# Kernel optimization log

Measured on AMD Instinct MI355X. Metric: run time of the kernel, lower is better.

## Reference

```python
import jax, jax.numpy as jnp
import numpy as np

B, IN, O = 256, 512, 10
STRUCTURES = list(range(32, 257, 32))  # 8 neuron structures
REPS, N_ACT = 4, 4


def _build_hidden_ids():
    ids = []
    i = 0
    # activation-major, then repetition, then structure (matches build_model_ids)
    for _ in range(N_ACT * REPS):
        for s in STRUCTURES:
            ids += [i] * s
            i += 1
    return np.asarray(ids, dtype=np.int32), i


def setup_inputs() -> dict:
    ids, M = _build_hidden_ids()
    H = len(ids)  # 18432
    k = jax.random.split(jax.random.key(0), 5)
    x = jax.random.normal(k[0], (B, IN), dtype=jnp.float32)
    hidden_w = jax.random.normal(k[1], (H, IN), dtype=jnp.float32) / np.sqrt(IN)
    hidden_b = jax.random.normal(k[2], (H,), dtype=jnp.float32) * 0.02
    out_w = jax.random.normal(k[3], (O, H), dtype=jnp.float32) * 0.05
    out_b = jax.random.normal(k[4], (M, O), dtype=jnp.float32) * 0.02
    return {"x": x, "hidden_w": hidden_w, "hidden_b": hidden_b,
            "out_w": out_w, "out_b": out_b,
            "hidden_ids": jnp.asarray(ids)}


_ACTS = [jax.nn.relu, jnp.tanh, jax.nn.sigmoid, lambda t: t]


def reference(x, hidden_w, hidden_b, out_w, out_b, hidden_ids):
    # hidden layer: [B, H]
    h = x @ hidden_w.T + hidden_b
    # per-activation contiguous splits (equal size H // n_act)
    chunks = jnp.split(h, N_ACT, axis=1)
    a = jnp.concatenate([f(c) for f, c in zip(_ACTS, chunks)], axis=1)  # [B, H]
    # per-hidden-neuron contribution to each output unit: [B, H, O]
    contrib = a[:, :, None] * out_w.T[None, :, :]
    M = out_b.shape[0]
    # segment-reduce hidden neurons into their model id: [M, B, O] -> [B, M, O]
    agg = jax.ops.segment_sum(contrib.transpose(1, 0, 2), hidden_ids, num_segments=M)
    return agg.transpose(1, 0, 2) + out_b[None, :, :]
```

## Files before the change

### kernel.cpp

```cpp
#include <hip/hip_runtime.h>
#include <hip/hip_bf16.h>

typedef __bf16 bf16x8 __attribute__((ext_vector_type(8)));
typedef float floatx4 __attribute__((ext_vector_type(4)));

#define BATCH 256
#define INDIM 512
#define ODIM 10
#define HTOT 18432
#define NMODEL 128
#define HTILE 64
#define BTILE 64
#define BK 32
#define ACT_CHUNK 4608
#define WCNT (HTOT * INDIM)
#define XCNT (BATCH * INDIM)
#define NJPG (HTOT / 32)

#define GLOAD_LDS(gp, lp) __builtin_amdgcn_global_load_lds( \
    (const __attribute__((address_space(1))) unsigned int*)(const void*)(gp), \
    (__attribute__((address_space(3))) unsigned int*)(lp), 16, 0, 0)

__device__ __forceinline__ unsigned pk2(float a, float b) {
    unsigned ua = __float_as_uint(a);
    ua = (ua + 0x7fffu + ((ua >> 16) & 1u)) >> 16;
    unsigned ub = __float_as_uint(b);
    ub = (ub + 0x7fffu + ((ub >> 16) & 1u)) >> 16;
    return ua | (ub << 16);
}

__device__ __forceinline__ float apply_act(float h, int aidx) {
    if (aidx == 0) return fmaxf(h, 0.f);
    if (aidx == 1) return 1.f - 2.f / (1.f + __expf(2.f * h));
    if (aidx == 2) return 1.f / (1.f + __expf(-h));
    return h;
}

__global__ __launch_bounds__(256) void convert_kernel(
    const float* __restrict__ hw, const float* __restrict__ x,
    unsigned short* __restrict__ dst)
{
    size_t i = (size_t)(blockIdx.x * 256 + threadIdx.x) * 8;
    const float* src = (i < (size_t)WCNT) ? hw + i : x + (i - WCNT);
    floatx4 v0 = *(const floatx4*)src;
    floatx4 v1 = *(const floatx4*)(src + 4);
    uint4 o;
    o.x = pk2(v0[0], v0[1]); o.y = pk2(v0[2], v0[3]);
    o.z = pk2(v1[0], v1[1]); o.w = pk2(v1[2], v1[3]);
    *(uint4*)(dst + i) = o;
}

__global__ __launch_bounds__(256, 5) void mlp_kernel(
    const unsigned short* __restrict__ wbf, const unsigned short* __restrict__ xbf,
    const float* __restrict__ hidden_b, const float* __restrict__ out_w,
    float* __restrict__ part)
{
    __shared__ __align__(16) unsigned short xs[BTILE * BK];
    __shared__ __align__(16) unsigned short wsx[HTILE * BK];
    __shared__ float wtile[ODIM * HTILE];
    __shared__ float btile[HTILE];

    const int tid = threadIdx.x;
    const int bid = blockIdx.x;
    const int jb = bid >> 2, bb = bid & 3;
    const int j0 = jb * HTILE;
    const int b0 = bb * BTILE;
    const int lane = tid & 63;
    const int wvid = tid >> 6;
    const int r = lane & 15;
    const int g = lane >> 4;

    for (int i = tid; i < ODIM * HTILE; i += 256)
        wtile[i] = out_w[(i >> 6) * HTOT + j0 + (i & 63)];
    if (tid < HTILE) btile[tid] = hidden_b[j0 + tid];

    floatx4 acc[4];
    #pragma unroll
    for (int jt = 0; jt < 4; jt++) acc[jt] = (floatx4)0.f;

    const int srow = wvid * 16 + (lane >> 2);
    const int scol = (lane & 3) * 8;
    const unsigned short* gw = wbf + (size_t)(j0 + srow) * INDIM + scol;
    const unsigned short* gx = xbf + (size_t)(b0 + srow) * INDIM + scol;
    unsigned short* lw = &wsx[wvid * 16 * BK];
    unsigned short* lx = &xs[wvid * 16 * BK];

    for (int kk = 0; kk < INDIM; kk += BK) {
        GLOAD_LDS(gw + kk, lw);
        GLOAD_LDS(gx + kk, lx);
        __syncthreads();
        bf16x8 bfr = *(const bf16x8*)&xs[(wvid * 16 + r) * BK + g * 8];
        #pragma unroll
        for (int jt = 0; jt < 4; jt++) {
            bf16x8 af = *(const bf16x8*)&wsx[(jt * 16 + r) * BK + g * 8];
            acc[jt] = __builtin_amdgcn_mfma_f32_16x16x32_bf16(af, bfr, acc[jt], 0, 0, 0);
        }
        __syncthreads();
    }

    const int aidx = j0 / ACT_CHUNK;
    const int b = b0 + wvid * 16 + r;

    #pragma unroll
    for (int jp = 0; jp < 2; jp++) {
        const int jpg = (j0 >> 5) + jp;
        float a[2][4];
        #pragma unroll
        for (int h = 0; h < 2; h++) {
            int jt = jp * 2 + h;
            #pragma unroll
            for (int q = 0; q < 4; q++)
                a[h][q] = apply_act(acc[jt][q] + btile[jt * 16 + g * 4 + q], aidx);
        }
        #pragma unroll
        for (int o = 0; o < ODIM; o++) {
            float p = 0.f;
            #pragma unroll
            for (int h = 0; h < 2; h++) {
                int jt = jp * 2 + h;
                const float* wr = &wtile[o * HTILE + jt * 16 + g * 4];
                p += a[h][0] * wr[0] + a[h][1] * wr[1] + a[h][2] * wr[2] + a[h][3] * wr[3];
            }
            p += __shfl_xor(p, 16, 64);
            p += __shfl_xor(p, 32, 64);
            if (lane < 16)
                part[((size_t)jpg * ODIM + o) * BATCH + b] = p;
        }
    }
}

__global__ __launch_bounds__(256) void finalize_kernel(
    const float* __restrict__ part, const float* __restrict__ out_b,
    float* __restrict__ out)
{
    const int mo = blockIdx.x;
    const int m = mo / ODIM, o = mo - m * ODIM;
    const int b = threadIdx.x;
    const int rep = m >> 3, idx = m & 7;
    const int jp0 = rep * 36 + (idx * (idx + 1)) / 2;
    const int cnt = idx + 1;

    float s = out_b[mo];
    for (int c = 0; c < cnt; c++)
        s += part[((size_t)(jp0 + c) * ODIM + o) * BATCH + b];
    out[((size_t)b * NMODEL + m) * ODIM + o] = s;
}

extern "C" void kernel_launch(void* const* d_in, const int* in_sizes, int n_in,
                              void* d_out, int out_size, void* d_ws, size_t ws_size,
                              hipStream_t stream) {
    const float* x   = (const float*)d_in[0];
    const float* hw  = (const float*)d_in[1];
    const float* hb  = (const float*)d_in[2];
    const float* ow  = (const float*)d_in[3];
    const float* ob  = (const float*)d_in[4];
    float* out = (float*)d_out;

    unsigned short* wbf = (unsigned short*)d_ws;
    unsigned short* xbf = wbf + WCNT;
    float* part = (float*)d_ws + (WCNT + XCNT) / 2;

    convert_kernel<<<(WCNT + XCNT) / 8 / 256, 256, 0, stream>>>(hw, x, wbf);
    mlp_kernel<<<(HTOT / HTILE) * (BATCH / BTILE), 256, 0, stream>>>(wbf, xbf, hb, ow, part);
    finalize_kernel<<<NMODEL * ODIM, 256, 0, stream>>>(part, ob, out);
}
```

Before: 115.9 us.

## Widen K tile, use 2x2 wave MFMA tiling and XOR-swizzled LDS layout

Raises the K step from 32 to 128, so the GEMM loop runs 4 iterations instead of 16 and barrier overhead drops. Each wave now owns a 32x32 sub-tile (2x2 MFMA fragments) instead of 16x64, which cuts LDS fragment reads per MFMA. A column XOR swizzle is applied to the global-to-LDS loads and reads to avoid bank conflicts. LDS use grows fourfold, and launch bounds drop to 4 blocks per CU, which may reduce occupancy.

```diff
diff --git a/kernel.cpp b/kernel.cpp
--- a/kernel.cpp
+++ b/kernel.cpp
@@ -11,7 +11,7 @@
 #define NMODEL 128
 #define HTILE 64
 #define BTILE 64
-#define BK 32
+#define BK 128
 #define ACT_CHUNK 4608
 #define WCNT (HTOT * INDIM)
 #define XCNT (BATCH * INDIM)
@@ -50,13 +50,13 @@
     *(uint4*)(dst + i) = o;
 }
 
-__global__ __launch_bounds__(256, 5) void mlp_kernel(
+__global__ __launch_bounds__(256, 4) void mlp_kernel(
     const unsigned short* __restrict__ wbf, const unsigned short* __restrict__ xbf,
     const float* __restrict__ hidden_b, const float* __restrict__ out_w,
     float* __restrict__ part)
 {
+    __shared__ __align__(16) unsigned short wsx[HTILE * BK];
     __shared__ __align__(16) unsigned short xs[BTILE * BK];
-    __shared__ __align__(16) unsigned short wsx[HTILE * BK];
     __shared__ float wtile[ODIM * HTILE];
     __shared__ float btile[HTILE];
 
@@ -67,6 +67,7 @@
     const int b0 = bb * BTILE;
     const int lane = tid & 63;
     const int wvid = tid >> 6;
+    const int jh = wvid >> 1, bh = wvid & 1;
     const int r = lane & 15;
     const int g = lane >> 4;
 
@@ -74,57 +75,81 @@
         wtile[i] = out_w[(i >> 6) * HTOT + j0 + (i & 63)];
     if (tid < HTILE) btile[tid] = hidden_b[j0 + tid];
 
-    floatx4 acc[4];
+    floatx4 acc[2][2];
     #pragma unroll
-    for (int jt = 0; jt < 4; jt++) acc[jt] = (floatx4)0.f;
+    for (int jt = 0; jt < 2; jt++)
+        #pragma unroll
+        for (int bt = 0; bt < 2; bt++) acc[jt][bt] = (floatx4)0.f;
 
-    const int srow = wvid * 16 + (lane >> 2);
-    const int scol = (lane & 3) * 8;
-    const unsigned short* gw = wbf + (size_t)(j0 + srow) * INDIM + scol;
-    const unsigned short* gx = xbf + (size_t)(b0 + srow) * INDIM + scol;
-    unsigned short* lw = &wsx[wvid * 16 * BK];
-    unsigned short* lx = &xs[wvid * 16 * BK];
+    const int drow = lane >> 4;
+    const int sc = lane & 15;
+    const unsigned short* gw[4];
+    const unsigned short* gx[4];
+    #pragma unroll
+    for (int i = 0; i < 4; i++) {
+        int row = wvid * 16 + i * 4 + drow;
+        int c = sc ^ (row & 7);
+        gw[i] = wbf + (size_t)(j0 + row) * INDIM + c * 8;
+        gx[i] = xbf + (size_t)(b0 + row) * INDIM + c * 8;
+    }
 
     for (int kk = 0; kk < INDIM; kk += BK) {
-        GLOAD_LDS(gw + kk, lw);
-        GLOAD_LDS(gx + kk, lx);
+        #pragma unroll
+        for (int i = 0; i < 4; i++) {
+            char* lw = (char*)wsx + (wvid * 16 + i * 4) * 256;
+            char* lx = (char*)xs  + (wvid * 16 + i * 4) * 256;
+            GLOAD_LDS(gw[i] + kk, lw);
+            GLOAD_LDS(gx[i] + kk, lx);
+        }
         __syncthreads();
-        bf16x8 bfr = *(const bf16x8*)&xs[(wvid * 16 + r) * BK + g * 8];
         #pragma unroll
-        for (int jt = 0; jt < 4; jt++) {
-            bf16x8 af = *(const bf16x8*)&wsx[(jt * 16 + r) * BK + g * 8];
-            acc[jt] = __builtin_amdgcn_mfma_f32_16x16x32_bf16(af, bfr, acc[jt], 0, 0, 0);
+        for (int s = 0; s < 4; s++) {
+            const int cx = (s * 4 + g) ^ (r & 7);
+            bf16x8 af[2], bfr[2];
+            #pragma unroll
+            for (int jt = 0; jt < 2; jt++)
+                af[jt] = *(const bf16x8*)&wsx[(jh * 32 + jt * 16 + r) * BK + cx * 8];
+            #pragma unroll
+            for (int bt = 0; bt < 2; bt++)
+                bfr[bt] = *(const bf16x8*)&xs[(bh * 32 + bt * 16 + r) * BK + cx * 8];
+            #pragma unroll
+            for (int jt = 0; jt < 2; jt++)
+                #pragma unroll
+                for (int bt = 0; bt < 2; bt++)
+                    acc[jt][bt] = __builtin_amdgcn_mfma_f32_16x16x32_bf16(af[jt], bfr[bt], acc[jt][bt], 0, 0, 0);
         }
         __syncthreads();
     }
 
     const int aidx = j0 / ACT_CHUNK;
-    const int b = b0 + wvid * 16 + r;
+    const int jpg = (j0 >> 5) + jh;
+
+    float a[2][2][4];
+    #pragma unroll
+    for (int jt = 0; jt < 2; jt++)
+        #pragma unroll
+        for (int bt = 0; bt < 2; bt++)
+            #pragma unroll
+            for (int q = 0; q < 4; q++)
+                a[jt][bt][q] = apply_act(acc[jt][bt][q] + btile[jh * 32 + jt * 16 + g * 4 + q], aidx);
 
     #pragma unroll
-    for (int jp = 0; jp < 2; jp++) {
-        const int jpg = (j0 >> 5) + jp;
-        float a[2][4];
+    for (int o = 0; o < ODIM; o++) {
         #pragma unroll
-        for (int h = 0; h < 2; h++) {
-            int jt = jp * 2 + h;
-            #pragma unroll
-            for (int q = 0; q < 4; q++)
-                a[h][q] = apply_act(acc[jt][q] + btile[jt * 16 + g * 4 + q], aidx);
-        }
-        #pragma unroll
-        for (int o = 0; o < ODIM; o++) {
+        for (int bt = 0; bt < 2; bt++) {
             float p = 0.f;
             #pragma unroll
-            for (int h = 0; h < 2; h++) {
-                int jt = jp * 2 + h;
-                const float* wr = &wtile[o * HTILE + jt * 16 + g * 4];
-                p += a[h][0] * wr[0] + a[h][1] * wr[1] + a[h][2] * wr[2] + a[h][3] * wr[3];
+            for (int jt = 0; jt < 2; jt++) {
+                const float* wr = &wtile[o * HTILE + jh * 32 + jt * 16 + g * 4];
+                p += a[jt][bt][0] * wr[0] + a[jt][bt][1] * wr[1]
+                   + a[jt][bt][2] * wr[2] + a[jt][bt][3] * wr[3];
             }
             p += __shfl_xor(p, 16, 64);
             p += __shfl_xor(p, 32, 64);
-            if (lane < 16)
+            if (lane < 16) {
+                int b = b0 + bh * 32 + bt * 16 + r;
                 part[((size_t)jpg * ODIM + o) * BATCH + b] = p;
+            }
         }
     }
 }
```

Result: no change. 117.3 us (+1.2%).
